# Performance work log

Hardware: AMD Instinct MI355X
Metric: run time of the kernel (lower is better)

Reference implementation:

```python
import jax, jax.numpy as jnp
import numpy as np

PATCH = 3
SIGMA2 = 0.5 ** 2
EPS = 1e-8


def _gauss_kernel():
    # depthwise Gaussian patch kernel, shape (6, 1, P, P, P), normalized to sum 1
    c = (PATCH - 1) / 2.0
    zz, yy, xx = np.meshgrid(np.arange(PATCH), np.arange(PATCH), np.arange(PATCH), indexing='ij')
    d2 = (xx - c) ** 2 + (yy - c) ** 2 + (zz - c) ** 2
    g = np.exp(-d2 / SIGMA2).astype(np.float32)
    g /= g.sum()
    k = np.zeros((6, 1, PATCH, PATCH, PATCH), np.float32)
    k[:, 0] = g
    return jnp.asarray(k)


def _shift(x, axis, step):
    # zero-padded shift: step=+1 -> out[i] = x[i+1]; step=-1 -> out[i] = x[i-1]
    n = x.shape[axis]
    pad = [(0, 0)] * x.ndim
    lo = 1 if step > 0 else 0
    pad[axis] = (0, 1) if step > 0 else (1, 0)
    xp = jnp.pad(x, pad)
    idx = [slice(None)] * x.ndim
    idx[axis] = slice(lo, lo + n)
    return xp[tuple(idx)]


def _mind(img):
    # shift-conv (one-hot 3x3x3 kernels) == 6 axis shifts: +z,-z,+y,-y,+x,-x
    shifted = jnp.concatenate([
        _shift(img, 2, 1), _shift(img, 2, -1),
        _shift(img, 3, 1), _shift(img, 3, -1),
        _shift(img, 4, 1), _shift(img, 4, -1),
    ], axis=1)                                  # (B,6,D,H,W)
    diff2 = (shifted - img) ** 2                # broadcast over channel dim
    gk = _gauss_kernel()
    Dp = jax.lax.conv_general_dilated(
        diff2, gk, window_strides=(1, 1, 1), padding='SAME',
        feature_group_count=6,
        dimension_numbers=('NCDHW', 'OIDHW', 'NCDHW'))  # depthwise Gaussian smoothing
    Vx = Dp.mean(axis=1, keepdims=True)
    num = jnp.exp(-Dp / (Vx + EPS))
    return num / (num.sum(axis=1, keepdims=True) + EPS)


def setup_inputs() -> dict:
    key = jax.random.key(0)
    img = jax.random.normal(key, (2, 1, 192, 192, 192), dtype=jnp.float32)
    return {"img": img}


def reference(img):
    return _mind(img)
```

## Files before the change

kernel.cpp:

```cpp
#include <hip/hip_runtime.h>

#define DHW 192
#define TX 32
#define TY 8
#define ZCH 32
#define NT (TX*TY)

#define RY  (TY+4)
#define RXW (TX+4)
#define EY  (TY+2)
#define EX  (TX+2)

__global__ __launch_bounds__(NT)
void mind3d_kernel(const float* __restrict__ img, float* __restrict__ out)
{
    __shared__ float ring[3][RY*RXW];
    __shared__ float Ebuf[6][EY*EX];
    __shared__ float Tbuf[6][EY*TX];

    const int tx  = threadIdx.x;
    const int ty  = threadIdx.y;
    const int tid = ty*TX + tx;

    const int x0 = blockIdx.x * TX;
    const int y0 = blockIdx.y * TY;
    const int zi = blockIdx.z;
    const int b  = zi / (DHW/ZCH);
    const int z0 = (zi - b*(DHW/ZCH)) * ZCH;

    const float* imgb = img + (size_t)b * ((size_t)DHW*DHW*DHW);

    const float a1    = 0.01831563889245986f;
    const float n1    = 1.0f/(1.0f + 2.0f*a1);
    const float norm3 = n1*n1*n1;

    float sm1[6], s0[6], sp1[6];
    #pragma unroll
    for (int c = 0; c < 6; ++c) { sm1[c] = 0.f; s0[c] = 0.f; }

    auto load_slice = [&](int z) {
        float* dst = ring[(z + 192) % 3];
        if (z < 0 || z >= DHW) {
            for (int i = tid; i < RY*RXW; i += NT) dst[i] = 0.f;
        } else {
            const float* sp = imgb + (size_t)z * (DHW*DHW);
            for (int i = tid; i < RY*RXW; i += NT) {
                int yy = i / RXW, xx = i - yy*RXW;
                int gy = y0 + yy - 2, gx = x0 + xx - 2;
                float v = 0.f;
                if ((unsigned)gy < (unsigned)DHW && (unsigned)gx < (unsigned)DHW)
                    v = sp[gy*DHW + gx];
                dst[i] = v;
            }
        }
    };

    load_slice(z0 - 2);
    load_slice(z0 - 1);

    for (int zs = z0 - 1; zs <= z0 + ZCH; ++zs) {
        load_slice(zs + 1);
        __syncthreads();

        const bool  zvalid = (zs >= 0 && zs < DHW);
        const float* rm = ring[(zs - 1 + 192) % 3];
        const float* rc = ring[(zs     + 192) % 3];
        const float* rp = ring[(zs + 1 + 192) % 3];

        if (zvalid) {
            for (int i = tid; i < EY*EX; i += NT) {
                int r = i / EX, px = i - r*EX;
                int gy = y0 + r - 1, gx = x0 + px - 1;
                int q  = (r + 1)*RXW + (px + 1);
                float c0 = rc[q];
                float e0=0.f,e1=0.f,e2=0.f,e3=0.f,e4=0.f,e5=0.f;
                if ((unsigned)gy < (unsigned)DHW && (unsigned)gx < (unsigned)DHW) {
                    float d;
                    d = rp[q]       - c0; e0 = d*d;
                    d = rm[q]       - c0; e1 = d*d;
                    d = rc[q + RXW] - c0; e2 = d*d;
                    d = rc[q - RXW] - c0; e3 = d*d;
                    d = rc[q + 1]   - c0; e4 = d*d;
                    d = rc[q - 1]   - c0; e5 = d*d;
                }
                Ebuf[0][i]=e0; Ebuf[1][i]=e1; Ebuf[2][i]=e2;
                Ebuf[3][i]=e3; Ebuf[4][i]=e4; Ebuf[5][i]=e5;
            }
        }
        __syncthreads();

        if (zvalid) {
            for (int i = tid; i < EY*TX; i += NT) {
                int r = i / TX, x = i - r*TX;
                int e = r*EX + x;
                #pragma unroll
                for (int c = 0; c < 6; ++c)
                    Tbuf[c][i] = a1*(Ebuf[c][e] + Ebuf[c][e + 2]) + Ebuf[c][e + 1];
            }
        }
        __syncthreads();

        #pragma unroll
        for (int c = 0; c < 6; ++c) {
            float s = 0.f;
            if (zvalid)
                s = a1*(Tbuf[c][ty*TX + tx] + Tbuf[c][(ty + 2)*TX + tx])
                    + Tbuf[c][(ty + 1)*TX + tx];
            sp1[c] = s;
        }

        const int zc = zs - 1;
        if (zc >= z0) {
            float dp[6], sum = 0.f;
            #pragma unroll
            for (int c = 0; c < 6; ++c) {
                dp[c] = norm3 * (a1*(sm1[c] + sp1[c]) + s0[c]);
                sum += dp[c];
            }
            float inv = 1.0f / (sum * (1.0f/6.0f) + 1e-8f);
            float num[6], nsum = 0.f;
            #pragma unroll
            for (int c = 0; c < 6; ++c) {
                num[c] = __expf(-dp[c] * inv);
                nsum += num[c];
            }
            float rs = 1.0f / (nsum + 1e-8f);
            size_t base = (((size_t)b*6)*DHW + zc) * ((size_t)DHW*DHW)
                        + (size_t)(y0 + ty)*DHW + (x0 + tx);
            #pragma unroll
            for (int c = 0; c < 6; ++c)
                out[base + (size_t)c * ((size_t)DHW*DHW*DHW)] = num[c] * rs;
        }

        #pragma unroll
        for (int c = 0; c < 6; ++c) { sm1[c] = s0[c]; s0[c] = sp1[c]; }
    }
}

extern "C" void kernel_launch(void* const* d_in, const int* in_sizes, int n_in,
                              void* d_out, int out_size, void* d_ws, size_t ws_size,
                              hipStream_t stream)
{
    const float* img = (const float*)d_in[0];
    float* out = (float*)d_out;
    dim3 block(TX, TY, 1);
    dim3 grid(DHW/TX, DHW/TY, 2*(DHW/ZCH));
    hipLaunchKernelGGL(mind3d_kernel, grid, block, 0, stream, img, out);
}
```

Baseline: 445.5 us.

## Rewrite MIND kernel with register-sliding y-window, float4 loads, 4-slice ring

Replaces the three-stage shared-memory pipeline (squared diffs, x-smoothing, y-smoothing) with per-thread register computation. Each thread handles 4 output rows and slides a window down y, computing diffs and the separable Gaussian smoothing in registers with edge masks. Slices are loaded with float4 into a 4-deep ring that prefetches two slices ahead, cutting the barriers to one per z step. Tile shape also changes to 64x16 with 16-deep z chunks. This removes shared-memory round trips and syncs at the cost of recomputing halo rows, more registers per thread, and a larger z halo per chunk.

```diff
diff --git a/kernel.cpp b/kernel.cpp
--- a/kernel.cpp
+++ b/kernel.cpp
@@ -1,139 +1,158 @@
 #include <hip/hip_runtime.h>
 
-#define DHW 192
-#define TX 32
-#define TY 8
-#define ZCH 32
-#define NT (TX*TY)
-
-#define RY  (TY+4)
-#define RXW (TX+4)
-#define EY  (TY+2)
-#define EX  (TX+2)
+#define DHW   192
+#define DHW2  (DHW*DHW)
+#define TX    64
+#define TTY   4
+#define YB    4
+#define BY    (TTY*YB)
+#define ZCH   16
+#define NT    (TX*TTY)
+#define RY    (BY+4)
+#define RXW   (TX+8)
+#define SLICE (RY*RXW)
+#define NF4   (SLICE/4)
+#define ROWF4 (RXW/4)
 
 __global__ __launch_bounds__(NT)
 void mind3d_kernel(const float* __restrict__ img, float* __restrict__ out)
 {
-    __shared__ float ring[3][RY*RXW];
-    __shared__ float Ebuf[6][EY*EX];
-    __shared__ float Tbuf[6][EY*TX];
+    __shared__ float ring[4][SLICE];
 
-    const int tx  = threadIdx.x;
-    const int ty  = threadIdx.y;
-    const int tid = ty*TX + tx;
+    const int lane = threadIdx.x;
+    const int ty   = threadIdx.y;
+    const int tid  = ty*TX + lane;
 
     const int x0 = blockIdx.x * TX;
-    const int y0 = blockIdx.y * TY;
+    const int y0 = blockIdx.y * BY;
     const int zi = blockIdx.z;
-    const int b  = zi / (DHW/ZCH);
-    const int z0 = (zi - b*(DHW/ZCH)) * ZCH;
+    const int nzc = DHW / ZCH;
+    const int b  = zi / nzc;
+    const int z0 = (zi - b*nzc) * ZCH;
 
-    const float* imgb = img + (size_t)b * ((size_t)DHW*DHW*DHW);
+    const float* imgb = img + (size_t)b * ((size_t)DHW * DHW2);
 
-    const float a1    = 0.01831563889245986f;
-    const float n1    = 1.0f/(1.0f + 2.0f*a1);
+    const float a1 = 0.01831563889245986f;
+    const float n1 = 1.0f/(1.0f + 2.0f*a1);
     const float norm3 = n1*n1*n1;
 
-    float sm1[6], s0[6], sp1[6];
-    #pragma unroll
-    for (int c = 0; c < 6; ++c) { sm1[c] = 0.f; s0[c] = 0.f; }
+    const int gx = x0 + lane;
+    const float mL = (gx == 0)     ? 0.f : 1.f;
+    const float mR = (gx == DHW-1) ? 0.f : 1.f;
+    const int wy = y0 + ty*YB;
+    const int u  = lane + 4;
 
     auto load_slice = [&](int z) {
-        float* dst = ring[(z + 192) % 3];
-        if (z < 0 || z >= DHW) {
-            for (int i = tid; i < RY*RXW; i += NT) dst[i] = 0.f;
+        float4* dst = (float4*)ring[(z + 8) & 3];
+        if ((unsigned)z >= (unsigned)DHW) {
+            for (int g = tid; g < NF4; g += NT)
+                dst[g] = float4{0.f, 0.f, 0.f, 0.f};
         } else {
-            const float* sp = imgb + (size_t)z * (DHW*DHW);
-            for (int i = tid; i < RY*RXW; i += NT) {
-                int yy = i / RXW, xx = i - yy*RXW;
-                int gy = y0 + yy - 2, gx = x0 + xx - 2;
-                float v = 0.f;
-                if ((unsigned)gy < (unsigned)DHW && (unsigned)gx < (unsigned)DHW)
-                    v = sp[gy*DHW + gx];
-                dst[i] = v;
+            const float* sp = imgb + (size_t)z * DHW2;
+            for (int g = tid; g < NF4; g += NT) {
+                int row = g / ROWF4;
+                int c4  = g - row*ROWF4;
+                int gy  = y0 - 2 + row;
+                int gxs = x0 - 16/4*4 + (c4 << 2) + (16/4*4 - 4);
+                float4 v = {0.f, 0.f, 0.f, 0.f};
+                if ((unsigned)gy < (unsigned)DHW && (unsigned)gxs <= (unsigned)(DHW - 4))
+                    v = *(const float4*)(sp + (size_t)gy*DHW + gxs);
+                dst[g] = v;
             }
         }
     };
 
+    float zm[YB][6], zc[YB][6];
+    #pragma unroll
+    for (int j = 0; j < YB; ++j)
+        #pragma unroll
+        for (int c = 0; c < 6; ++c) { zm[j][c] = 0.f; zc[j][c] = 0.f; }
+
     load_slice(z0 - 2);
     load_slice(z0 - 1);
+    load_slice(z0);
+    __syncthreads();
 
     for (int zs = z0 - 1; zs <= z0 + ZCH; ++zs) {
-        load_slice(zs + 1);
-        __syncthreads();
+        if (zs < z0 + ZCH) load_slice(zs + 2);
 
-        const bool  zvalid = (zs >= 0 && zs < DHW);
-        const float* rm = ring[(zs - 1 + 192) % 3];
-        const float* rc = ring[(zs     + 192) % 3];
-        const float* rp = ring[(zs + 1 + 192) % 3];
+        const bool zok = ((unsigned)zs < (unsigned)DHW);
+        const float* rcs = ring[(zs + 8) & 3] + ty*YB*RXW + u;
+        const float* rps = ring[(zs + 9) & 3] + (ty*YB + 1)*RXW + u;
+        const float* rms = ring[(zs + 7) & 3] + (ty*YB + 1)*RXW + u;
 
-        if (zvalid) {
-            for (int i = tid; i < EY*EX; i += NT) {
-                int r = i / EX, px = i - r*EX;
-                int gy = y0 + r - 1, gx = x0 + px - 1;
-                int q  = (r + 1)*RXW + (px + 1);
-                float c0 = rc[q];
-                float e0=0.f,e1=0.f,e2=0.f,e3=0.f,e4=0.f,e5=0.f;
-                if ((unsigned)gy < (unsigned)DHW && (unsigned)gx < (unsigned)DHW) {
-                    float d;
-                    d = rp[q]       - c0; e0 = d*d;
-                    d = rm[q]       - c0; e1 = d*d;
-                    d = rc[q + RXW] - c0; e2 = d*d;
-                    d = rc[q - RXW] - c0; e3 = d*d;
-                    d = rc[q + 1]   - c0; e4 = d*d;
-                    d = rc[q - 1]   - c0; e5 = d*d;
+        float A0,A1,A2,A3,A4, B0,B1,B2,B3,B4;
+        A0 = rcs[-2];     A1 = rcs[-1];     A2 = rcs[0];   A3 = rcs[1];     A4 = rcs[2];
+        B0 = rcs[RXW-2];  B1 = rcs[RXW-1];  B2 = rcs[RXW]; B3 = rcs[RXW+1]; B4 = rcs[RXW+2];
+
+        float T[3][6];
+        const int zcout = zs - 1;
+        const bool emitz = (zcout >= z0);
+
+        #pragma unroll
+        for (int k = 0; k < 6; ++k) {
+            const int gr = wy - 1 + k;
+            const float* rk = rcs + (k + 2)*RXW;
+            float C0 = rk[-2], C1 = rk[-1], C2 = rk[0], C3 = rk[1], C4 = rk[2];
+            const float* pk = rps + k*RXW;
+            const float* mk = rms + k*RXW;
+            float zpL = pk[-1], zpC = pk[0], zpR = pk[1];
+            float zmL = mk[-1], zmC = mk[0], zmR = mk[1];
+
+            const bool rok = zok && ((unsigned)gr < (unsigned)DHW);
+            if (rok) {
+                float d0 = B1-B0, d1 = B2-B1, d2 = B3-B2, d3 = B4-B3;
+                float q0 = d0*d0, q1 = d1*d1, q2 = d2*d2, q3 = d3*d3;
+                float eL, eC, eR;
+                eL = zpL-B1; eC = zpC-B2; eR = zpR-B3;
+                T[k%3][0] = a1*(eL*eL*mL + eR*eR*mR) + eC*eC;
+                eL = zmL-B1; eC = zmC-B2; eR = zmR-B3;
+                T[k%3][1] = a1*(eL*eL*mL + eR*eR*mR) + eC*eC;
+                eL = C1-B1;  eC = C2-B2;  eR = C3-B3;
+                T[k%3][2] = a1*(eL*eL*mL + eR*eR*mR) + eC*eC;
+                eL = A1-B1;  eC = A2-B2;  eR = A3-B3;
+                T[k%3][3] = a1*(eL*eL*mL + eR*eR*mR) + eC*eC;
+                T[k%3][4] = a1*(q1*mL + q3*mR) + q2;
+                T[k%3][5] = a1*(q0*mL + q2*mR) + q1;
+            } else {
+                #pragma unroll
+                for (int c = 0; c < 6; ++c) T[k%3][c] = 0.f;
+            }
+
+            if (k >= 2) {
+                const int j = k - 2;
+                float sp_[6];
+                #pragma unroll
+                for (int c = 0; c < 6; ++c)
+                    sp_[c] = a1*(T[(k-2)%3][c] + T[k%3][c]) + T[(k-1)%3][c];
+                if (emitz) {
+                    float dp[6], sum = 0.f;
+                    #pragma unroll
+                    for (int c = 0; c < 6; ++c) {
+                        dp[c] = norm3 * (a1*(zm[j][c] + sp_[c]) + zc[j][c]);
+                        sum += dp[c];
+                    }
+                    float inv = 1.0f / (sum * (1.0f/6.0f) + 1e-8f);
+                    float num[6], nsum = 0.f;
+                    #pragma unroll
+                    for (int c = 0; c < 6; ++c) {
+                        num[c] = __expf(-dp[c] * inv);
+                        nsum += num[c];
+                    }
+                    float rs = 1.0f / (nsum + 1e-8f);
+                    size_t base = ((size_t)(6*b)*DHW + zcout) * (size_t)DHW2
+                                + (size_t)(wy + j)*DHW + (size_t)gx;
+                    #pragma unroll
+                    for (int c = 0; c < 6; ++c)
+                        out[base + (size_t)c * ((size_t)DHW*DHW2)] = num[c]*rs;
                 }
-                Ebuf[0][i]=e0; Ebuf[1][i]=e1; Ebuf[2][i]=e2;
-                Ebuf[3][i]=e3; Ebuf[4][i]=e4; Ebuf[5][i]=e5;
+                #pragma unroll
+                for (int c = 0; c < 6; ++c) { zm[j][c] = zc[j][c]; zc[j][c] = sp_[c]; }
             }
+            A0=B0; A1=B1; A2=B2; A3=B3; A4=B4;
+            B0=C0; B1=C1; B2=C2; B3=C3; B4=C4;
         }
         __syncthreads();
-
-        if (zvalid) {
-            for (int i = tid; i < EY*TX; i += NT) {
-                int r = i / TX, x = i - r*TX;
-                int e = r*EX + x;
-                #pragma unroll
-                for (int c = 0; c < 6; ++c)
-                    Tbuf[c][i] = a1*(Ebuf[c][e] + Ebuf[c][e + 2]) + Ebuf[c][e + 1];
-            }
-        }
-        __syncthreads();
-
-        #pragma unroll
-        for (int c = 0; c < 6; ++c) {
-            float s = 0.f;
-            if (zvalid)
-                s = a1*(Tbuf[c][ty*TX + tx] + Tbuf[c][(ty + 2)*TX + tx])
-                    + Tbuf[c][(ty + 1)*TX + tx];
-            sp1[c] = s;
-        }
-
-        const int zc = zs - 1;
-        if (zc >= z0) {
-            float dp[6], sum = 0.f;
-            #pragma unroll
-            for (int c = 0; c < 6; ++c) {
-                dp[c] = norm3 * (a1*(sm1[c] + sp1[c]) + s0[c]);
-                sum += dp[c];
-            }
-            float inv = 1.0f / (sum * (1.0f/6.0f) + 1e-8f);
-            float num[6], nsum = 0.f;
-            #pragma unroll
-            for (int c = 0; c < 6; ++c) {
-                num[c] = __expf(-dp[c] * inv);
-                nsum += num[c];
-            }
-            float rs = 1.0f / (nsum + 1e-8f);
-            size_t base = (((size_t)b*6)*DHW + zc) * ((size_t)DHW*DHW)
-                        + (size_t)(y0 + ty)*DHW + (x0 + tx);
-            #pragma unroll
-            for (int c = 0; c < 6; ++c)
-                out[base + (size_t)c * ((size_t)DHW*DHW*DHW)] = num[c] * rs;
-        }
-
-        #pragma unroll
-        for (int c = 0; c < 6; ++c) { sm1[c] = s0[c]; s0[c] = sp1[c]; }
     }
 }
 
@@ -143,7 +162,7 @@
 {
     const float* img = (const float*)d_in[0];
     float* out = (float*)d_out;
-    dim3 block(TX, TY, 1);
-    dim3 grid(DHW/TX, DHW/TY, 2*(DHW/ZCH));
+    dim3 block(TX, TTY, 1);
+    dim3 grid(DHW/TX, DHW/BY, 2*(DHW/ZCH));
     hipLaunchKernelGGL(mind3d_kernel, grid, block, 0, stream, img, out);
 }
```

After: 423.0 us. 1.05x faster.
